# Optimization experiments

Hardware: AMD Instinct MI355X
Metric: run time of the kernel (lower is better)

## Reference

```python
import jax, jax.numpy as jnp
import numpy as np

N = 50000          # num nodes
NUM_HE = 10000     # num hyperedges
E = 800000         # num graph edges
INC = 800000       # num (node, hyperedge) incidences
IN_C, HID, OUT_C = 128, 128, 64
SLOPE = 0.01       # torch leaky_relu default negative slope


def _leaky(x):
    return jnp.where(x >= 0, x, SLOPE * x)


def hypergraph_conv(x, he_index, theta, bias):
    # PyG HypergraphConv (no attention, unit hyperedge weights):
    # out = D^{-1} H B^{-1} H^T (X Theta) + bias
    node_idx, he_idx = he_index[0], he_index[1]
    x = x @ theta                                            # [N, F]
    ones = jnp.ones(node_idx.shape[0], x.dtype)
    D = jax.ops.segment_sum(ones, node_idx, num_segments=N)           # node degree
    B = jax.ops.segment_sum(ones, he_idx, num_segments=NUM_HE)        # hyperedge degree
    Dinv = jnp.where(D > 0, 1.0 / D, 0.0)
    Binv = jnp.where(B > 0, 1.0 / B, 0.0)
    # node -> hyperedge
    m = jax.ops.segment_sum(x[node_idx], he_idx, num_segments=NUM_HE) * Binv[:, None]
    # hyperedge -> node
    out = jax.ops.segment_sum(m[he_idx], node_idx, num_segments=N) * Dinv[:, None]
    return out + bias


def graph_conv(x, edge_index, w_rel, b_rel, w_root):
    # PyG GraphConv (aggr='add'): out_i = W_rel * sum_{j->i} x_j + b_rel + W_root * x_i
    src, dst = edge_index[0], edge_index[1]
    agg = jax.ops.segment_sum(x[src], dst, num_segments=N)
    return agg @ w_rel + b_rel + x @ w_root


def _forward(X, edge_index, hyperedge_index,
             hc1_w, hc1_b, lin1_w, lin1_b,
             hc2_w, hc2_b, lin2_w, lin2_b,
             c1_wrel, c1_brel, c1_wroot, glin1_w, glin1_b,
             c2_wrel, c2_brel, c2_wroot, glin2_w, glin2_b,
             fc_w, fc_b):
    # dropout is identity in eval mode (and first two calls in the source discard their output)
    X = _leaky(hypergraph_conv(X, hyperedge_index, hc1_w, hc1_b) + (X @ lin1_w + lin1_b))
    X = _leaky(hypergraph_conv(X, hyperedge_index, hc2_w, hc2_b) + (X @ lin2_w + lin2_b))
    X = _leaky(graph_conv(X, edge_index, c1_wrel, c1_brel, c1_wroot) + (X @ glin1_w + glin1_b))
    X = _leaky(graph_conv(X, edge_index, c2_wrel, c2_brel, c2_wroot) + (X @ glin2_w + glin2_b))
    y = X @ fc_w + fc_b
    return X, y


def setup_inputs() -> dict:
    key = jax.random.key(0)
    ks = jax.random.split(key, 32)
    s = 0.02
    inp = {
        'X': jax.random.normal(ks[0], (N, IN_C), jnp.float32),
        'edge_index': jnp.stack([
            jax.random.randint(ks[1], (E,), 0, N),
            jax.random.randint(ks[2], (E,), 0, N)]).astype(jnp.int64),
        'hyperedge_index': jnp.stack([
            jax.random.randint(ks[3], (INC,), 0, N),
            jax.random.randint(ks[4], (INC,), 0, NUM_HE)]).astype(jnp.int64),
        'hc1_w': jax.random.normal(ks[5], (IN_C, HID), jnp.float32) * s,
        'hc1_b': jnp.zeros((HID,), jnp.float32),
        'lin1_w': jax.random.normal(ks[6], (IN_C, HID), jnp.float32) * s,
        'lin1_b': jnp.zeros((HID,), jnp.float32),
        'hc2_w': jax.random.normal(ks[7], (HID, HID), jnp.float32) * s,
        'hc2_b': jnp.zeros((HID,), jnp.float32),
        'lin2_w': jax.random.normal(ks[8], (HID, HID), jnp.float32) * s,
        'lin2_b': jnp.zeros((HID,), jnp.float32),
        'c1_wrel': jax.random.normal(ks[9], (HID, HID), jnp.float32) * s,
        'c1_brel': jnp.zeros((HID,), jnp.float32),
        'c1_wroot': jax.random.normal(ks[10], (HID, HID), jnp.float32) * s,
        'glin1_w': jax.random.normal(ks[11], (HID, HID), jnp.float32) * s,
        'glin1_b': jnp.zeros((HID,), jnp.float32),
        'c2_wrel': jax.random.normal(ks[12], (HID, HID), jnp.float32) * s,
        'c2_brel': jnp.zeros((HID,), jnp.float32),
        'c2_wroot': jax.random.normal(ks[13], (HID, HID), jnp.float32) * s,
        'glin2_w': jax.random.normal(ks[14], (HID, HID), jnp.float32) * s,
        'glin2_b': jnp.zeros((HID,), jnp.float32),
        'fc_w': jax.random.normal(ks[15], (HID, OUT_C), jnp.float32) * s,
        'fc_b': jnp.zeros((OUT_C,), jnp.float32),
    }
    return inp


def reference(X, edge_index, hyperedge_index,
              hc1_w, hc1_b, lin1_w, lin1_b,
              hc2_w, hc2_b, lin2_w, lin2_b,
              c1_wrel, c1_brel, c1_wroot, glin1_w, glin1_b,
              c2_wrel, c2_brel, c2_wroot, glin2_w, glin2_b,
              fc_w, fc_b):
    return _forward(X, edge_index, hyperedge_index,
                    hc1_w, hc1_b, lin1_w, lin1_b,
                    hc2_w, hc2_b, lin2_w, lin2_b,
                    c1_wrel, c1_brel, c1_wroot, glin1_w, glin1_b,
                    c2_wrel, c2_brel, c2_wroot, glin2_w, glin2_b,
                    fc_w, fc_b)
```

## Files before the change

kernel.cpp:

```cpp
#include <hip/hip_runtime.h>

#define NN 50000
#define HECNT 10000
#define EE 800000
#define II 800000
#define NBK 128
#define CHUNK 4096
#define BKCAP 8192
#define BIN_GRID ((EE + CHUNK - 1) / CHUNK)

typedef _Float16 half8 __attribute__((ext_vector_type(8)));
typedef float f32x4    __attribute__((ext_vector_type(4)));
typedef unsigned short u16;

__device__ __forceinline__ void task_info(int t, int& n, int& cbase, int& obase) {
    if (t == 0)      { n = HECNT; cbase = 0;           obase = 0; }
    else if (t == 1) { n = NN;    cbase = HECNT;       obase = HECNT + 1; }
    else             { n = NN;    cbase = HECNT + NN;  obase = HECNT + NN + 2; }
}

__global__ __launch_bounds__(256) void prep_k(const int* __restrict__ EIX, const int* __restrict__ HIX,
                                              int* __restrict__ flags, int* __restrict__ bcur,
                                              const float* __restrict__ hc1_w, const float* __restrict__ lin1_w,
                                              const float* __restrict__ hc2_w, const float* __restrict__ lin2_w,
                                              const float* __restrict__ c1_wrel, const float* __restrict__ c1_wroot,
                                              const float* __restrict__ glin1_w,
                                              const float* __restrict__ c2_wrel, const float* __restrict__ c2_wroot,
                                              const float* __restrict__ glin2_w,
                                              const float* __restrict__ fc_w,
                                              _Float16* __restrict__ F) {
    int set = blockIdx.y;
    int tid = threadIdx.x;
    if (set == 5) {
        if (blockIdx.x != 0) return;
        for (int i = tid; i < 3 * NBK; i += 256) bcur[i] = i * BKCAP;
        __shared__ int o0, o1;
        if (tid == 0) { o0 = 0; o1 = 0; }
        __syncthreads();
        atomicOr(&o0, EIX[2 * tid + 1]);
        atomicOr(&o1, HIX[2 * tid + 1]);
        __syncthreads();
        if (tid == 0) { flags[0] = (o0 == 0); flags[1] = (o1 == 0); }
        return;
    }
    int nfrag = (set == 4) ? 1024 : 4096;
    int NT = (set < 2) ? 16 : (set == 4 ? 4 : 8);
    int fid = blockIdx.x * 256 + tid;
    if (fid >= nfrag) return;
    int lane = fid & 63;
    int tile = fid >> 6;
    int nt = tile % NT, ks = tile / NT;
    int n = nt * 16 + (lane & 15);
    int kbase = ks * 32 + (lane >> 4) * 8;
    _Float16* dst = F + (size_t)set * 32768 + (size_t)fid * 8;
    #pragma unroll
    for (int j = 0; j < 8; j++) {
        int k = kbase + j;
        float w;
        if (set == 0)      w = (n < 128) ? hc1_w[k * 128 + n] : lin1_w[k * 128 + n - 128];
        else if (set == 1) w = (n < 128) ? hc2_w[k * 128 + n] : lin2_w[k * 128 + n - 128];
        else if (set == 2) w = (k < 128) ? c1_wrel[k * 128 + n]
                                         : c1_wroot[(k - 128) * 128 + n] + glin1_w[(k - 128) * 128 + n];
        else if (set == 3) w = (k < 128) ? c2_wrel[k * 128 + n]
                                         : c2_wroot[(k - 128) * 128 + n] + glin2_w[(k - 128) * 128 + n];
        else               w = fc_w[k * 64 + n];
        dst[j] = (_Float16)w;
    }
}

__device__ void bin_body(int bx, int t,
                         const int* __restrict__ EIX, const int* __restrict__ HIX,
                         const int* __restrict__ flags, int* __restrict__ bcur,
                         unsigned* __restrict__ pairs) {
    __shared__ int hcnt[NBK], hrun[NBK], gbase[NBK];
    int tid = threadIdx.x;
    int n, cb, ob; task_info(t, n, cb, ob);
    int span = (n + NBK - 1) / NBK;
    long long base = (long long)bx * CHUNK;
    int f = (t == 2) ? flags[0] : flags[1];
    const int* arr = (t == 2) ? EIX : HIX;
    int mul = f ? 2 : 1;
    const int* row1 = arr + (size_t)mul * 800000;
    const int* darr = (t == 1) ? arr : row1;
    const int* varr = (t == 1) ? row1 : arr;
    int rng = (t == 0) ? HECNT : NN;

    for (int i = tid; i < NBK; i += 256) { hcnt[i] = 0; hrun[i] = 0; }
    __syncthreads();

    int d[16], v[16];
    #pragma unroll
    for (int jj = 0; jj < 8; jj++) {
        long long i = base + jj * 512 + tid * 2;
        int d0 = -1, d1 = -1, v0 = 0, v1 = 0;
        if (i < EE) {
            if (f) {
                int4 dw = *(const int4*)(darr + 2 * i);
                int4 vw = *(const int4*)(varr + 2 * i);
                d0 = dw.x; d1 = dw.z; v0 = vw.x; v1 = vw.z;
            } else {
                int2 dw = *(const int2*)(darr + i);
                int2 vw = *(const int2*)(varr + i);
                d0 = dw.x; d1 = dw.y; v0 = vw.x; v1 = vw.y;
            }
            if ((unsigned)d0 >= (unsigned)rng || (unsigned)v0 >= 65536u) d0 = -1;
            if ((unsigned)d1 >= (unsigned)rng || (unsigned)v1 >= 65536u) d1 = -1;
        }
        d[2 * jj] = d0; v[2 * jj] = v0;
        d[2 * jj + 1] = d1; v[2 * jj + 1] = v1;
        if (d0 >= 0) atomicAdd(&hcnt[d0 / span], 1);
        if (d1 >= 0) atomicAdd(&hcnt[d1 / span], 1);
    }
    __syncthreads();

    if (tid < NBK) gbase[tid] = hcnt[tid] ? atomicAdd(&bcur[t * NBK + tid], hcnt[tid]) : 0;
    __syncthreads();

    #pragma unroll
    for (int j = 0; j < 16; j++) {
        if (d[j] >= 0) {
            int b = d[j] / span;
            int p = gbase[b] + atomicAdd(&hrun[b], 1);
            if (p < (t * NBK + b + 1) * BKCAP)
                pairs[p] = ((unsigned)d[j] << 16) | (unsigned)v[j];
        }
    }
}

__device__ void gemm2_f32(int bx, const float* __restrict__ A,
                          const half8* __restrict__ Bf,
                          const float* __restrict__ b2,
                          _Float16* __restrict__ O1, _Float16* __restrict__ O2, int M) {
    constexpr int K = 128, NT = 16;
    int tid = threadIdx.x;
    int wave = tid >> 6, lane = tid & 63;
    int quad = lane >> 4, l16 = lane & 15;
    int rowbase = bx * 64 + wave * 16;
    int row = rowbase + l16;

    f32x4 acc[NT];
    f32x4 zero4 = {0.f, 0.f, 0.f, 0.f};
    #pragma unroll
    for (int nt = 0; nt < NT; nt++) acc[nt] = zero4;

    #pragma unroll
    for (int ks = 0; ks < 4; ks++) {
        int k0 = ks * 32 + quad * 8;
        half8 af = {0, 0, 0, 0, 0, 0, 0, 0};
        if (row < M) {
            const float* ap = A + (size_t)row * K + k0;
            float4 x0 = *(const float4*)ap;
            float4 x1 = *(const float4*)(ap + 4);
            af = half8{(_Float16)x0.x, (_Float16)x0.y, (_Float16)x0.z, (_Float16)x0.w,
                       (_Float16)x1.x, (_Float16)x1.y, (_Float16)x1.z, (_Float16)x1.w};
        }
        #pragma unroll
        for (int nt = 0; nt < NT; nt++) {
            half8 bfr = Bf[(ks * NT + nt) * 64 + lane];
            acc[nt] = __builtin_amdgcn_mfma_f32_16x16x32_f16(af, bfr, acc[nt], 0, 0, 0);
        }
    }

    #pragma unroll
    for (int nt = 0; nt < NT; nt++) {
        int col = nt * 16 + l16;
        bool second = (col >= 128);
        int c = second ? col - 128 : col;
        float bv = second ? b2[c] : 0.f;
        _Float16* O = second ? O2 : O1;
        #pragma unroll
        for (int r = 0; r < 4; r++) {
            int rr = rowbase + quad * 4 + r;
            if (rr < M) O[(size_t)rr * 128 + c] = (_Float16)(acc[nt][r] + bv);
        }
    }
}

__global__ __launch_bounds__(256) void phase1_k(const int* __restrict__ EIX, const int* __restrict__ HIX,
                                                const int* __restrict__ flags, int* __restrict__ bcur,
                                                unsigned* __restrict__ pairs,
                                                const float* __restrict__ X, const half8* __restrict__ F0,
                                                const float* __restrict__ lin1_b,
                                                _Float16* __restrict__ P, _Float16* __restrict__ L) {
    int bx = blockIdx.x;
    if (bx < 3 * BIN_GRID) {
        bin_body(bx % BIN_GRID, bx / BIN_GRID, EIX, HIX, flags, bcur, pairs);
    } else {
        gemm2_f32(bx - 3 * BIN_GRID, X, F0, lin1_b, P, L, NN);
    }
}

__global__ __launch_bounds__(256) void bfin2_k(const int* __restrict__ bcur,
                                               const unsigned* __restrict__ pairs,
                                               int* __restrict__ offs,
                                               u16* __restrict__ vals) {
    int idx = blockIdx.x;
    int t = idx / NBK, b = idx % NBK;
    int n, cb, ob; task_info(t, n, cb, ob);
    int span = (n + NBK - 1) / NBK;
    int dlo = min(b * span, n), dhi = min(dlo + span, n);
    int tid = threadIdx.x;
    int lane = tid & 63, w = tid >> 6;

    __shared__ int scnt[NBK];
    __shared__ int wtot[2];
    {
        int s = 0;
        if (tid < NBK) {
            int c = bcur[t * NBK + tid] - (t * NBK + tid) * BKCAP;
            s = max(0, min(c, BKCAP));
            #pragma unroll
            for (int o = 1; o < 64; o <<= 1) {
                int u = __shfl_up(s, o, 64);
                if (lane >= o) s += u;
            }
            if (lane == 63) wtot[w] = s;
        }
        __syncthreads();
        if (tid < NBK) {
            if (w == 1) s += wtot[0];
            scnt[tid] = s;
        }
        __syncthreads();
    }
    if (b == NBK - 1 && tid == 0) offs[ob + n] = scnt[NBK - 1];
    if (dhi <= dlo) return;
    int nd = dhi - dlo;
    int base = (b > 0) ? scnt[b - 1] : 0;
    int cnt = scnt[b] - base;

    __shared__ int hist[512], cur[512];
    __shared__ u16 win[BKCAP];
    __shared__ int wsum[4];
    for (int i = tid; i < 512; i += 256) hist[i] = 0;
    __syncthreads();

    const unsigned* pw = pairs + (size_t)idx * BKCAP;
    for (int i = tid; i < cnt; i += 256) {
        int dl = (int)(pw[i] >> 16) - dlo;
        if ((unsigned)dl < (unsigned)nd) atomicAdd(&hist[dl], 1);
    }
    __syncthreads();

    int i0 = 2 * tid, i1 = 2 * tid + 1;
    int ha = hist[i0], hb = hist[i1];
    int s = ha + hb;
    #pragma unroll
    for (int o = 1; o < 64; o <<= 1) {
        int u = __shfl_up(s, o, 64);
        if (lane >= o) s += u;
    }
    if (lane == 63) wsum[w] = s;
    __syncthreads();
    int woff = 0;
    #pragma unroll
    for (int k = 0; k < 4; k++) woff += (k < w) ? wsum[k] : 0;
    int incl1 = woff + s;
    int incl0 = incl1 - hb;
    if (i0 < nd) { int ex = incl0 - ha; offs[ob + dlo + i0] = base + ex; cur[i0] = ex; }
    if (i1 < nd) { int ex = incl1 - hb; offs[ob + dlo + i1] = base + ex; cur[i1] = ex; }
    __syncthreads();

    for (int i = tid; i < cnt; i += 256) {
        unsigned pv = pw[i];
        int dl = (int)(pv >> 16) - dlo;
        if ((unsigned)dl < (unsigned)nd) {
            int p = atomicAdd(&cur[dl], 1);
            if ((unsigned)p < (unsigned)BKCAP) win[p] = (u16)(pv & 0xffffu);
        }
    }
    __syncthreads();
    u16* vw = vals + (size_t)t * 800000 + base;
    for (int i = tid; i < cnt; i += 256) vw[i] = win[i];
}

__global__ __launch_bounds__(256) void gather_k(const int* __restrict__ offs,
                                                const u16* __restrict__ vals,
                                                const _Float16* __restrict__ src,
                                                _Float16* __restrict__ out,
                                                int ndst, int nsrc, int scale_flag,
                                                const float* __restrict__ bias,
                                                const _Float16* __restrict__ addend,
                                                int act) {
    int wave = threadIdx.x >> 6, lane = threadIdx.x & 63;
    int sub = lane >> 4, l16 = lane & 15;
    int d = blockIdx.x * 4 + wave;
    if (d >= ndst) return;
    int beg = offs[d], end = offs[d + 1];
    int f = l16 * 8;
    float a[8] = {0.f, 0.f, 0.f, 0.f, 0.f, 0.f, 0.f, 0.f};
    auto acc_row = [&](int s) {
        if ((unsigned)s < (unsigned)nsrc) {
            half8 u = *(const half8*)(src + (size_t)s * 128 + f);
            #pragma unroll
            for (int j = 0; j < 8; j++) a[j] += (float)u[j];
        }
    };
    int e = beg + sub;
    for (; e + 28 < end; e += 32) {
        int s0 = vals[e], s1 = vals[e + 4], s2 = vals[e + 8], s3 = vals[e + 12];
        int s4 = vals[e + 16], s5 = vals[e + 20], s6 = vals[e + 24], s7 = vals[e + 28];
        acc_row(s0); acc_row(s1); acc_row(s2); acc_row(s3);
        acc_row(s4); acc_row(s5); acc_row(s6); acc_row(s7);
    }
    for (; e + 12 < end; e += 16) {
        int s0 = vals[e], s1 = vals[e + 4], s2 = vals[e + 8], s3 = vals[e + 12];
        acc_row(s0); acc_row(s1); acc_row(s2); acc_row(s3);
    }
    for (; e < end; e += 4) acc_row(vals[e]);
    #pragma unroll
    for (int j = 0; j < 8; j++) {
        a[j] += __shfl_xor(a[j], 16, 64);
        a[j] += __shfl_xor(a[j], 32, 64);
    }
    if (sub == 0) {
        if (scale_flag) {
            int c = end - beg;
            float iv = (c > 0) ? 1.f / (float)c : 0.f;
            #pragma unroll
            for (int j = 0; j < 8; j++) a[j] *= iv;
        }
        if (bias) {
            f32x4 b0 = *(const f32x4*)(bias + f);
            f32x4 b1 = *(const f32x4*)(bias + f + 4);
            #pragma unroll
            for (int j = 0; j < 4; j++) { a[j] += b0[j]; a[4 + j] += b1[j]; }
        }
        if (addend) {
            half8 u = *(const half8*)(addend + (size_t)d * 128 + f);
            #pragma unroll
            for (int j = 0; j < 8; j++) a[j] += (float)u[j];
        }
        if (act) {
            #pragma unroll
            for (int j = 0; j < 8; j++) a[j] = (a[j] >= 0.f) ? a[j] : 0.01f * a[j];
        }
        half8 o;
        #pragma unroll
        for (int j = 0; j < 8; j++) o[j] = (_Float16)a[j];
        *(half8*)(out + (size_t)d * 128 + f) = o;
    }
}

__global__ __launch_bounds__(256) void gemm2h_k(const _Float16* __restrict__ A,
                                                const half8* __restrict__ Bf,
                                                const float* __restrict__ b2,
                                                _Float16* __restrict__ O1,
                                                _Float16* __restrict__ O2,
                                                int M) {
    constexpr int K = 128, NT = 16;
    int tid = threadIdx.x;
    int wave = tid >> 6, lane = tid & 63;
    int quad = lane >> 4, l16 = lane & 15;
    int rowbase = blockIdx.x * 64 + wave * 16;
    int row = rowbase + l16;

    f32x4 acc[NT];
    f32x4 zero4 = {0.f, 0.f, 0.f, 0.f};
    #pragma unroll
    for (int nt = 0; nt < NT; nt++) acc[nt] = zero4;

    #pragma unroll
    for (int ks = 0; ks < 4; ks++) {
        int k0 = ks * 32 + quad * 8;
        half8 af = {0, 0, 0, 0, 0, 0, 0, 0};
        if (row < M) af = *(const half8*)(A + (size_t)row * K + k0);
        #pragma unroll
        for (int nt = 0; nt < NT; nt++) {
            half8 bfr = Bf[(ks * NT + nt) * 64 + lane];
            acc[nt] = __builtin_amdgcn_mfma_f32_16x16x32_f16(af, bfr, acc[nt], 0, 0, 0);
        }
    }

    #pragma unroll
    for (int nt = 0; nt < NT; nt++) {
        int col = nt * 16 + l16;
        bool second = (col >= 128);
        int c = second ? col - 128 : col;
        float bv = second ? b2[c] : 0.f;
        _Float16* O = second ? O2 : O1;
        #pragma unroll
        for (int r = 0; r < 4; r++) {
            int rr = rowbase + quad * 4 + r;
            if (rr < M) O[(size_t)rr * 128 + c] = (_Float16)(acc[nt][r] + bv);
        }
    }
}

template <int FC>
__global__ __launch_bounds__(256) void gemmk2_k(const _Float16* __restrict__ A0,
                                                const _Float16* A1,
                                                const half8* __restrict__ Bf,
                                                const float* __restrict__ brel,
                                                const float* __restrict__ blin,
                                                float* __restrict__ Cf,
                                                _Float16* Ch,
                                                const half8* __restrict__ Bfc,
                                                const float* __restrict__ bfc,
                                                float* __restrict__ Y,
                                                int M) {
    __shared__ __align__(16) _Float16 lt[64 * 136];
    constexpr int NT = 8;
    int tid = threadIdx.x;
    int wave = tid >> 6, lane = tid & 63;
    int quad = lane >> 4, l16 = lane & 15;
    int rowbase = blockIdx.x * 64 + wave * 16;
    int row = rowbase + l16;

    f32x4 acc[NT];
    f32x4 zero4 = {0.f, 0.f, 0.f, 0.f};
    #pragma unroll
    for (int nt = 0; nt < NT; nt++) acc[nt] = zero4;

    #pragma unroll
    for (int ks = 0; ks < 8; ks++) {
        int k0 = ks * 32 + quad * 8;
        const _Float16* Asel = (k0 < 128) ? A0 : A1;
        int ka = k0 & 127;
        half8 af = {0, 0, 0, 0, 0, 0, 0, 0};
        if (row < M) af = *(const half8*)(Asel + (size_t)row * 128 + ka);
        #pragma unroll
        for (int nt = 0; nt < NT; nt++) {
            half8 bfr = Bf[(ks * NT + nt) * 64 + lane];
            acc[nt] = __builtin_amdgcn_mfma_f32_16x16x32_f16(af, bfr, acc[nt], 0, 0, 0);
        }
    }

    #pragma unroll
    for (int nt = 0; nt < NT; nt++) {
        int col = nt * 16 + l16;
        float bv = brel[col] + blin[col];
        #pragma unroll
        for (int r = 0; r < 4; r++) {
            int rr = rowbase + quad * 4 + r;
            float v = acc[nt][r] + bv;
            v = (v >= 0.f) ? v : 0.01f * v;
            if (rr < M) {
                if (FC) Cf[(size_t)rr * 128 + col] = v;
                else    Ch[(size_t)rr * 128 + col] = (_Float16)v;
            }
            if (FC) lt[(wave * 16 + quad * 4 + r) * 136 + col] = (_Float16)v;
        }
    }

    if (FC) {
        f32x4 a2[4];
        #pragma unroll
        for (int nt = 0; nt < 4; nt++) a2[nt] = zero4;
        #pragma unroll
        for (int ks = 0; ks < 4; ks++) {
            half8 af = *(const half8*)(lt + (wave * 16 + l16) * 136 + ks * 32 + quad * 8);
            #pragma unroll
            for (int nt = 0; nt < 4; nt++) {
                half8 bfr = Bfc[(ks * 4 + nt) * 64 + lane];
                a2[nt] = __builtin_amdgcn_mfma_f32_16x16x32_f16(af, bfr, a2[nt], 0, 0, 0);
            }
        }
        #pragma unroll
        for (int nt = 0; nt < 4; nt++) {
            int col = nt * 16 + l16;
            float bv = bfc[col];
            #pragma unroll
            for (int r = 0; r < 4; r++) {
                int rr = rowbase + quad * 4 + r;
                if (rr < M) Y[(size_t)rr * 64 + col] = a2[nt][r] + bv;
            }
        }
    }
}

extern "C" void kernel_launch(void* const* d_in, const int* in_sizes, int n_in,
                              void* d_out, int out_size, void* d_ws, size_t ws_size,
                              hipStream_t stream) {
    const float* X       = (const float*)d_in[0];
    const int*   EIX     = (const int*)d_in[1];
    const int*   HIX     = (const int*)d_in[2];
    const float* hc1_w   = (const float*)d_in[3];
    const float* hc1_b   = (const float*)d_in[4];
    const float* lin1_w  = (const float*)d_in[5];
    const float* lin1_b  = (const float*)d_in[6];
    const float* hc2_w   = (const float*)d_in[7];
    const float* hc2_b   = (const float*)d_in[8];
    const float* lin2_w  = (const float*)d_in[9];
    const float* lin2_b  = (const float*)d_in[10];
    const float* c1_wrel = (const float*)d_in[11];
    const float* c1_brel = (const float*)d_in[12];
    const float* c1_wroot= (const float*)d_in[13];
    const float* glin1_w = (const float*)d_in[14];
    const float* glin1_b = (const float*)d_in[15];
    const float* c2_wrel = (const float*)d_in[16];
    const float* c2_brel = (const float*)d_in[17];
    const float* c2_wroot= (const float*)d_in[18];
    const float* glin2_w = (const float*)d_in[19];
    const float* glin2_b = (const float*)d_in[20];
    const float* fc_w    = (const float*)d_in[21];
    const float* fc_b    = (const float*)d_in[22];

    char* wsp = (char*)d_ws;
    size_t off = 0;
    auto carve = [&](size_t bytes) -> char* {
        char* p = wsp + off;
        off = (off + bytes + 255) & ~(size_t)255;
        return p;
    };
    int*   flags  = (int*)carve(16);
    int*   offs   = (int*)carve(110003 * 4);
    int*   bcur   = (int*)carve(3 * NBK * 4);
    u16*   vals   = (u16*)carve(2400000 * 2);
    _Float16* F   = (_Float16*)carve((4 * 32768 + 8192) * 2);
    unsigned* pairs = (unsigned*)carve((size_t)3 * NBK * BKCAP * 4);
    _Float16* P  = (_Float16*)carve((size_t)NN * 128 * 2);
    _Float16* L  = (_Float16*)carve((size_t)NN * 128 * 2);
    _Float16* MH = (_Float16*)carve((size_t)HECNT * 128 * 2);
    _Float16* XA = (_Float16*)carve((size_t)NN * 128 * 2);

    float* XO = (float*)d_out;
    float* YO = XO + (size_t)NN * 128;

    const half8* F0 = (const half8*)F;
    const half8* F1 = (const half8*)(F + 32768);
    const half8* F2 = (const half8*)(F + 2 * 32768);
    const half8* F3 = (const half8*)(F + 3 * 32768);
    const half8* F4 = (const half8*)(F + 4 * 32768);

    const int* offs_he   = offs;
    const int* offs_node = offs + HECNT + 1;
    const int* offs_dst  = offs + HECNT + NN + 2;
    const u16* vals_he   = vals;
    const u16* vals_node = vals + 800000;
    const u16* vals_dst  = vals + 1600000;

    int g64 = (NN + 63) / 64;
    int ghe = (HECNT + 3) / 4;
    int gnn = (NN + 3) / 4;

    prep_k<<<dim3(16, 6), 256, 0, stream>>>(EIX, HIX, flags, bcur,
                                            hc1_w, lin1_w, hc2_w, lin2_w,
                                            c1_wrel, c1_wroot, glin1_w,
                                            c2_wrel, c2_wroot, glin2_w, fc_w, F);
    phase1_k<<<3 * BIN_GRID + g64, 256, 0, stream>>>(EIX, HIX, flags, bcur, pairs,
                                                     X, F0, lin1_b, P, L);
    bfin2_k<<<3 * NBK, 256, 0, stream>>>(bcur, pairs, offs, vals);

    gather_k<<<ghe, 256, 0, stream>>>(offs_he, vals_he, P, MH, HECNT, NN, 1, nullptr, nullptr, 0);
    gather_k<<<gnn, 256, 0, stream>>>(offs_node, vals_node, MH, XA, NN, HECNT, 1, hc1_b, L, 1);

    gemm2h_k<<<g64, 256, 0, stream>>>(XA, F1, lin2_b, P, L, NN);
    gather_k<<<ghe, 256, 0, stream>>>(offs_he, vals_he, P, MH, HECNT, NN, 1, nullptr, nullptr, 0);
    gather_k<<<gnn, 256, 0, stream>>>(offs_node, vals_node, MH, XA, NN, HECNT, 1, hc2_b, L, 1);

    gather_k<<<gnn, 256, 0, stream>>>(offs_dst, vals_dst, XA, P, NN, NN, 0, nullptr, nullptr, 0);
    gemmk2_k<0><<<g64, 256, 0, stream>>>(P, XA, F2, c1_brel, glin1_b,
                                         nullptr, XA, nullptr, nullptr, nullptr, NN);

    gather_k<<<gnn, 256, 0, stream>>>(offs_dst, vals_dst, XA, P, NN, NN, 0, nullptr, nullptr, 0);
    gemmk2_k<1><<<g64, 256, 0, stream>>>(P, XA, F3, c2_brel, glin2_b,
                                         XO, nullptr, F4, fc_b, YO, NN);
}
```

Measured before the change: 443.0 us.

## Merge hyperedge-index binning passes and pad bucket cursors to separate cache lines

The two binning tasks that both read the hyperedge incidence array (bin by hyperedge and bin by node) now run in one block, so HIX is loaded once and both histograms are built together. This cuts the binning grid from three chunk sets to two. Global bucket cursors are spaced 32 ints apart so that atomics on different buckets do not land on the same cache line. The cost is more shared memory and registers per binning block, and the padding enlarges the cursor array.

```diff
diff --git a/kernel.cpp b/kernel.cpp
--- a/kernel.cpp
+++ b/kernel.cpp
@@ -7,6 +7,7 @@
 #define NBK 128
 #define CHUNK 4096
 #define BKCAP 8192
+#define BCSTRIDE 32
 #define BIN_GRID ((EE + CHUNK - 1) / CHUNK)
 
 typedef _Float16 half8 __attribute__((ext_vector_type(8)));
@@ -33,7 +34,7 @@
     int tid = threadIdx.x;
     if (set == 5) {
         if (blockIdx.x != 0) return;
-        for (int i = tid; i < 3 * NBK; i += 256) bcur[i] = i * BKCAP;
+        for (int i = tid; i < 3 * NBK; i += 256) bcur[i * BCSTRIDE] = i * BKCAP;
         __shared__ int o0, o1;
         if (tid == 0) { o0 = 0; o1 = 0; }
         __syncthreads();
@@ -68,22 +69,91 @@
     }
 }
 
-__device__ void bin_body(int bx, int t,
-                         const int* __restrict__ EIX, const int* __restrict__ HIX,
-                         const int* __restrict__ flags, int* __restrict__ bcur,
-                         unsigned* __restrict__ pairs) {
+__device__ void bin_hix(int bx,
+                        const int* __restrict__ HIX,
+                        const int* __restrict__ flags, int* __restrict__ bcur,
+                        unsigned* __restrict__ pairs) {
+    __shared__ int hcnt[2][NBK], hrun[2][NBK], gbase[2][NBK];
+    int tid = threadIdx.x;
+    const int span0 = (HECNT + NBK - 1) / NBK;
+    const int span1 = (NN + NBK - 1) / NBK;
+    long long base = (long long)bx * CHUNK;
+    int f = flags[1];
+    int mul = f ? 2 : 1;
+    const int* narr = HIX;
+    const int* harr = HIX + (size_t)mul * 800000;
+
+    for (int i = tid; i < NBK; i += 256) {
+        hcnt[0][i] = 0; hrun[0][i] = 0;
+        hcnt[1][i] = 0; hrun[1][i] = 0;
+    }
+    __syncthreads();
+
+    int nd[16], he[16];
+    #pragma unroll
+    for (int jj = 0; jj < 8; jj++) {
+        long long i = base + jj * 512 + tid * 2;
+        int n0 = -1, n1 = -1, h0 = -1, h1 = -1;
+        if (i < II) {
+            if (f) {
+                int4 nw = *(const int4*)(narr + 2 * i);
+                int4 hw = *(const int4*)(harr + 2 * i);
+                n0 = nw.x; n1 = nw.z; h0 = hw.x; h1 = hw.z;
+            } else {
+                int2 nw = *(const int2*)(narr + i);
+                int2 hw = *(const int2*)(harr + i);
+                n0 = nw.x; n1 = nw.y; h0 = hw.x; h1 = hw.y;
+            }
+        }
+        nd[2 * jj] = n0; he[2 * jj] = h0;
+        nd[2 * jj + 1] = n1; he[2 * jj + 1] = h1;
+        if ((unsigned)h0 < (unsigned)HECNT && (unsigned)n0 < 65536u) atomicAdd(&hcnt[0][h0 / span0], 1);
+        if ((unsigned)h1 < (unsigned)HECNT && (unsigned)n1 < 65536u) atomicAdd(&hcnt[0][h1 / span0], 1);
+        if ((unsigned)n0 < (unsigned)NN && (unsigned)h0 < 65536u) atomicAdd(&hcnt[1][n0 / span1], 1);
+        if ((unsigned)n1 < (unsigned)NN && (unsigned)h1 < 65536u) atomicAdd(&hcnt[1][n1 / span1], 1);
+    }
+    __syncthreads();
+
+    if (tid < NBK) {
+        int c = hcnt[0][tid];
+        gbase[0][tid] = c ? atomicAdd(&bcur[tid * BCSTRIDE], c) : 0;
+    } else if (tid < 2 * NBK) {
+        int b = tid - NBK;
+        int c = hcnt[1][b];
+        gbase[1][b] = c ? atomicAdd(&bcur[(NBK + b) * BCSTRIDE], c) : 0;
+    }
+    __syncthreads();
+
+    #pragma unroll
+    for (int j = 0; j < 16; j++) {
+        int n = nd[j], h = he[j];
+        if ((unsigned)h < (unsigned)HECNT && (unsigned)n < 65536u) {
+            int b = h / span0;
+            int p = gbase[0][b] + atomicAdd(&hrun[0][b], 1);
+            if (p < (b + 1) * BKCAP)
+                pairs[p] = ((unsigned)h << 16) | (unsigned)n;
+        }
+        if ((unsigned)n < (unsigned)NN && (unsigned)h < 65536u) {
+            int b = n / span1;
+            int p = gbase[1][b] + atomicAdd(&hrun[1][b], 1);
+            if (p < (NBK + b + 1) * BKCAP)
+                pairs[p] = ((unsigned)n << 16) | (unsigned)h;
+        }
+    }
+}
+
+__device__ void bin_eix(int bx,
+                        const int* __restrict__ EIX,
+                        const int* __restrict__ flags, int* __restrict__ bcur,
+                        unsigned* __restrict__ pairs) {
     __shared__ int hcnt[NBK], hrun[NBK], gbase[NBK];
     int tid = threadIdx.x;
-    int n, cb, ob; task_info(t, n, cb, ob);
-    int span = (n + NBK - 1) / NBK;
+    const int span = (NN + NBK - 1) / NBK;
     long long base = (long long)bx * CHUNK;
-    int f = (t == 2) ? flags[0] : flags[1];
-    const int* arr = (t == 2) ? EIX : HIX;
+    int f = flags[0];
     int mul = f ? 2 : 1;
-    const int* row1 = arr + (size_t)mul * 800000;
-    const int* darr = (t == 1) ? arr : row1;
-    const int* varr = (t == 1) ? row1 : arr;
-    int rng = (t == 0) ? HECNT : NN;
+    const int* darr = EIX + (size_t)mul * 800000;
+    const int* varr = EIX;
 
     for (int i = tid; i < NBK; i += 256) { hcnt[i] = 0; hrun[i] = 0; }
     __syncthreads();
@@ -103,8 +173,8 @@
                 int2 vw = *(const int2*)(varr + i);
                 d0 = dw.x; d1 = dw.y; v0 = vw.x; v1 = vw.y;
             }
-            if ((unsigned)d0 >= (unsigned)rng || (unsigned)v0 >= 65536u) d0 = -1;
-            if ((unsigned)d1 >= (unsigned)rng || (unsigned)v1 >= 65536u) d1 = -1;
+            if ((unsigned)d0 >= (unsigned)NN || (unsigned)v0 >= 65536u) d0 = -1;
+            if ((unsigned)d1 >= (unsigned)NN || (unsigned)v1 >= 65536u) d1 = -1;
         }
         d[2 * jj] = d0; v[2 * jj] = v0;
         d[2 * jj + 1] = d1; v[2 * jj + 1] = v1;
@@ -113,7 +183,7 @@
     }
     __syncthreads();
 
-    if (tid < NBK) gbase[tid] = hcnt[tid] ? atomicAdd(&bcur[t * NBK + tid], hcnt[tid]) : 0;
+    if (tid < NBK) gbase[tid] = hcnt[tid] ? atomicAdd(&bcur[(2 * NBK + tid) * BCSTRIDE], hcnt[tid]) : 0;
     __syncthreads();
 
     #pragma unroll
@@ -121,7 +191,7 @@
         if (d[j] >= 0) {
             int b = d[j] / span;
             int p = gbase[b] + atomicAdd(&hrun[b], 1);
-            if (p < (t * NBK + b + 1) * BKCAP)
+            if (p < (2 * NBK + b + 1) * BKCAP)
                 pairs[p] = ((unsigned)d[j] << 16) | (unsigned)v[j];
         }
     }
@@ -183,10 +253,12 @@
                                                 const float* __restrict__ lin1_b,
                                                 _Float16* __restrict__ P, _Float16* __restrict__ L) {
     int bx = blockIdx.x;
-    if (bx < 3 * BIN_GRID) {
-        bin_body(bx % BIN_GRID, bx / BIN_GRID, EIX, HIX, flags, bcur, pairs);
+    if (bx < BIN_GRID) {
+        bin_hix(bx, HIX, flags, bcur, pairs);
+    } else if (bx < 2 * BIN_GRID) {
+        bin_eix(bx - BIN_GRID, EIX, flags, bcur, pairs);
     } else {
-        gemm2_f32(bx - 3 * BIN_GRID, X, F0, lin1_b, P, L, NN);
+        gemm2_f32(bx - 2 * BIN_GRID, X, F0, lin1_b, P, L, NN);
     }
 }
 
@@ -207,7 +279,7 @@
     {
         int s = 0;
         if (tid < NBK) {
-            int c = bcur[t * NBK + tid] - (t * NBK + tid) * BKCAP;
+            int c = bcur[(t * NBK + tid) * BCSTRIDE] - (t * NBK + tid) * BKCAP;
             s = max(0, min(c, BKCAP));
             #pragma unroll
             for (int o = 1; o < 64; o <<= 1) {
@@ -505,7 +577,7 @@
     };
     int*   flags  = (int*)carve(16);
     int*   offs   = (int*)carve(110003 * 4);
-    int*   bcur   = (int*)carve(3 * NBK * 4);
+    int*   bcur   = (int*)carve(3 * NBK * BCSTRIDE * 4);
     u16*   vals   = (u16*)carve(2400000 * 2);
     _Float16* F   = (_Float16*)carve((4 * 32768 + 8192) * 2);
     unsigned* pairs = (unsigned*)carve((size_t)3 * NBK * BKCAP * 4);
@@ -538,7 +610,7 @@
                                             hc1_w, lin1_w, hc2_w, lin2_w,
                                             c1_wrel, c1_wroot, glin1_w,
                                             c2_wrel, c2_wroot, glin2_w, fc_w, F);
-    phase1_k<<<3 * BIN_GRID + g64, 256, 0, stream>>>(EIX, HIX, flags, bcur, pairs,
+    phase1_k<<<2 * BIN_GRID + g64, 256, 0, stream>>>(EIX, HIX, flags, bcur, pairs,
                                                      X, F0, lin1_b, P, L);
     bfin2_k<<<3 * NBK, 256, 0, stream>>>(bcur, pairs, offs, vals);
 
```

After: 444.8 us. Within noise of the previous version (+0.4%).
